# Optimization experiments

Measured on AMD Instinct MI355X. Metric: run time of the kernel, lower is better.

## Reference

```python
import math
import jax, jax.numpy as jnp
import numpy as np

PHI = (1.0 + math.sqrt(5.0)) / 2.0
B, S, E, H, L = 2, 2048, 1024, 16, 5
DH = E // H


def setup_inputs() -> dict:
    key = jax.random.key(0)
    ks = jax.random.split(key, 16)
    rn = lambda k, sh, sc=0.02: jax.random.normal(k, sh, jnp.float32) * sc
    return {
        'x': jax.random.normal(ks[0], (B, S, E), jnp.float32),
        'consciousness_levels': jax.random.uniform(ks[1], (B, H), jnp.float32),
        'Wc': rn(ks[2], (L, E, E)), 'bc': jnp.zeros((L, E), jnp.float32),
        'Wf': rn(ks[3], (L, E, H)), 'bf': jnp.zeros((L, H), jnp.float32),
        'Wq': rn(ks[4], (E, E)), 'bq': jnp.zeros((E,), jnp.float32),
        'Wk': rn(ks[5], (E, E)), 'bk': jnp.zeros((E,), jnp.float32),
        'Wv': rn(ks[6], (E, E)), 'bv': jnp.zeros((E,), jnp.float32),
        'Wo': rn(ks[7], (E, E)), 'bo': jnp.zeros((E,), jnp.float32),
        'Wc1': rn(ks[8], (2 * DH, E)), 'bc1': jnp.zeros((E,), jnp.float32),
        'Wc2': rn(ks[9], (E, 1)), 'bc2': jnp.zeros((1,), jnp.float32),
        'gate': jax.random.normal(ks[10], (L, H), jnp.float32) / math.sqrt(H),
        'phi_phase': PHI * jnp.arange(H, dtype=jnp.float32),
        'ln_g': jnp.ones((E,), jnp.float32), 'ln_b': jnp.zeros((E,), jnp.float32),
    }


def reference(x, consciousness_levels, Wc, bc, Wf, bf, Wq, bq, Wk, bk, Wv, bv,
              Wo, bo, Wc1, bc1, Wc2, bc2, gate, phi_phase, ln_g, ln_b):
    b, s, e = x.shape
    l, _, h = Wf.shape
    dh = e // h
    # per-level consciousness scalar: consciousness_levels[:, level % num_heads] -> [B, L]
    cl = consciousness_levels[:, jnp.arange(l) % h]
    # consciousness-enhanced features: mean over L of (x @ Wc_l + bc_l) * cl[:, l]
    feat = jnp.einsum('bse,leo->lbso', x, Wc) + bc[:, None, None, :]   # [L,B,S,E]
    ce = jnp.mean(feat * cl.T[:, :, None, None], axis=0)                # [B,S,E]
    # QKV projections (spectral_norm linears; normalized weights supplied directly)
    Q = (ce @ Wq + bq).reshape(b, s, h, dh).transpose(0, 2, 1, 3)       # [B,H,S,Dh]
    K = (ce @ Wk + bk).reshape(b, s, h, dh).transpose(0, 2, 1, 3)
    V = (ce @ Wv + bv).reshape(b, s, h, dh).transpose(0, 2, 1, 3)
    scores = jnp.einsum('bhsd,bhtd->bhst', Q, K) / math.sqrt(dh)        # [B,H,S,S]
    # phi-harmonic phase modulation (scalar per (B,H), averaged over levels)
    pooled = ce.mean(axis=1)                                            # [B,E]
    freq = jnp.einsum('be,leh->lbh', pooled, Wf) + bf[:, None, :]       # [L,B,H]
    phase = jnp.sin(phi_phase[None, None, :] * freq * cl.T[:, :, None]).mean(axis=0)  # [B,H]
    scores = scores + 0.1 * phase[:, :, None, None]
    # quantum coherence gate per (B,H): sigmoid MLP on pooled Q/K head features
    ci = jnp.concatenate([Q.mean(axis=2), K.mean(axis=2)], axis=-1)     # [B,H,2*Dh]
    cw = jax.nn.sigmoid(jax.nn.gelu(ci @ Wc1 + bc1, approximate=False) @ Wc2 + bc2)  # [B,H,1]
    scores = scores * (1.0 + cw[..., None])
    aw = jax.nn.softmax(scores, axis=-1)
    # consciousness gating on attention weights, then re-softmax
    gw = jax.nn.softmax(gate, axis=1)                                   # [L,H]
    factor = jnp.prod(1.0 + 0.1 * cl[:, :, None] * gw[None, :, :], axis=1)  # [B,H]
    aw = jax.nn.softmax(aw * factor[:, :, None, None], axis=-1)
    attended = jnp.einsum('bhst,bhtd->bhsd', aw, V)
    out = attended.transpose(0, 2, 1, 3).reshape(b, s, e) @ Wo + bo
    y = x + out  # dropout is identity in eval
    mu = y.mean(axis=-1, keepdims=True)
    var = ((y - mu) ** 2).mean(axis=-1, keepdims=True)
    return (y - mu) / jnp.sqrt(var + 1e-5) * ln_g + ln_b
```

## Files before the change

### kernel.cpp

```cpp
#include <hip/hip_runtime.h>
#include <math.h>

#define BB 2
#define SS 2048
#define EE 1024
#define HH 16
#define LL 5
#define DH 64
#define QS (3 * 1024)

typedef __attribute__((ext_vector_type(8))) short bf16x8;
typedef __attribute__((ext_vector_type(4))) float f32x4;

__device__ __forceinline__ unsigned short f2bf(float f) {
  unsigned u = __float_as_uint(f);
  u += 0x7fffu + ((u >> 16) & 1u);
  return (unsigned short)(u >> 16);
}
__device__ __forceinline__ float bf2f(unsigned short u) {
  return __uint_as_float((unsigned)u << 16);
}
__device__ __forceinline__ f32x4 mfma16(bf16x8 a, bf16x8 b, f32x4 c) {
  return __builtin_amdgcn_mfma_f32_16x16x32_bf16(a, b, c, 0, 0, 0);
}
__device__ __forceinline__ unsigned cvtpk(float a, float b) {
  unsigned r;
  asm("v_cvt_pk_bf16_f32 %0, %1, %2" : "=v"(r) : "v"(a), "v"(b));
  return r;
}
__device__ __forceinline__ void gload16(const unsigned short* g, unsigned short* l) {
  __builtin_amdgcn_global_load_lds(
      (const __attribute__((address_space(1))) void*)g,
      (__attribute__((address_space(3))) void*)l, 16, 0, 0);
}

__global__ void prep_pack(const float* __restrict__ cons, const float* __restrict__ gate,
                          const float* __restrict__ bc,
                          const float* __restrict__ bq, const float* __restrict__ bk,
                          const float* __restrict__ bv,
                          float* __restrict__ beff, float* __restrict__ bqkv,
                          float* __restrict__ factor) {
  int i = blockIdx.x * 256 + threadIdx.x;
  if (i == 0) {
    float gw[LL][HH];
    for (int l = 0; l < LL; ++l) {
      float mx = -1e30f;
      for (int h = 0; h < HH; ++h) mx = fmaxf(mx, gate[l * HH + h]);
      float s = 0.f;
      for (int h = 0; h < HH; ++h) { gw[l][h] = expf(gate[l * HH + h] - mx); s += gw[l][h]; }
      for (int h = 0; h < HH; ++h) gw[l][h] /= s;
    }
    for (int b = 0; b < BB; ++b)
      for (int h = 0; h < HH; ++h) {
        float f = 1.f;
        for (int l = 0; l < LL; ++l) f *= 1.f + 0.1f * cons[b * HH + l] * gw[l][h];
        factor[b * HH + h] = f;
      }
  }
  if (i < BB * EE) {
    int b = i >> 10, e = i & 1023;
    float a = 0.f;
    #pragma unroll
    for (int l = 0; l < LL; ++l) a += cons[b * HH + l] * bc[l * EE + e];
    beff[i] = a * (1.f / LL);
  } else {
    int j = i - BB * EE;
    float v = (j < EE) ? bq[j] : (j < 2 * EE) ? bk[j - EE] : bv[j - 2 * EE];
    bqkv[j] = v;
  }
}

__global__ __launch_bounds__(256) void wceffT_kernel(const float* __restrict__ Wc,
                                                     const float* __restrict__ cons,
                                                     unsigned short* __restrict__ Wt) {
  int o0 = blockIdx.x * 64, e0 = blockIdx.y * 64, b = blockIdx.z;
  __shared__ float t[64][69];
  int tid = threadIdx.x;
  float w[LL];
  #pragma unroll
  for (int l = 0; l < LL; ++l) w[l] = cons[b * HH + l] * (1.f / LL);
  #pragma unroll
  for (int i = 0; i < 4; ++i) {
    int idx = tid + i * 256;
    int r = idx >> 4, c4 = idx & 15;
    float4 acc = {0.f, 0.f, 0.f, 0.f};
    #pragma unroll
    for (int l = 0; l < LL; ++l) {
      float4 v = *(const float4*)&Wc[(long)l * EE * EE + (long)(e0 + r) * EE + o0 + c4 * 4];
      acc.x += w[l] * v.x; acc.y += w[l] * v.y; acc.z += w[l] * v.z; acc.w += w[l] * v.w;
    }
    t[r][c4 * 4 + 0] = acc.x; t[r][c4 * 4 + 1] = acc.y;
    t[r][c4 * 4 + 2] = acc.z; t[r][c4 * 4 + 3] = acc.w;
  }
  __syncthreads();
  #pragma unroll
  for (int i = 0; i < 2; ++i) {
    int idx = tid + i * 256;
    int o = idx >> 3, ech = idx & 7;
    unsigned short u[8];
    #pragma unroll
    for (int j = 0; j < 8; ++j) u[j] = f2bf(t[ech * 8 + j][o]);
    unsigned short* dst = Wt + (long)b * EE * EE + (long)(o0 + o) * EE + e0 + ech * 8;
    *(ushort4*)&dst[0] = *(ushort4*)&u[0];
    *(ushort4*)&dst[4] = *(ushort4*)&u[4];
  }
}

__global__ __launch_bounds__(256) void wT4_kernel(
    const float* __restrict__ W0, const float* __restrict__ W1,
    const float* __restrict__ W2, const float* __restrict__ W3,
    unsigned short* __restrict__ Wqkvt, unsigned short* __restrict__ Wot) {
  int z = blockIdx.z;
  const float* W = (z == 0) ? W0 : (z == 1) ? W1 : (z == 2) ? W2 : W3;
  unsigned short* Wt = (z < 3) ? (Wqkvt + (size_t)z * EE * EE) : Wot;
  int o0 = blockIdx.x * 64, e0 = blockIdx.y * 64;
  __shared__ float t[64][69];
  int tid = threadIdx.x;
  #pragma unroll
  for (int i = 0; i < 4; ++i) {
    int idx = tid + i * 256;
    int r = idx >> 4, c4 = idx & 15;
    float4 v = *(const float4*)&W[(long)(e0 + r) * EE + o0 + c4 * 4];
    t[r][c4 * 4 + 0] = v.x; t[r][c4 * 4 + 1] = v.y;
    t[r][c4 * 4 + 2] = v.z; t[r][c4 * 4 + 3] = v.w;
  }
  __syncthreads();
  #pragma unroll
  for (int i = 0; i < 2; ++i) {
    int idx = tid + i * 256;
    int o = idx >> 3, ech = idx & 7;
    unsigned short u[8];
    #pragma unroll
    for (int j = 0; j < 8; ++j) u[j] = f2bf(t[ech * 8 + j][o]);
    unsigned short* dst = Wt + (long)(o0 + o) * EE + e0 + ech * 8;
    *(ushort4*)&dst[0] = *(ushort4*)&u[0];
    *(ushort4*)&dst[4] = *(ushort4*)&u[4];
  }
}

__global__ void cvt_bf_kernel(const float* __restrict__ in, unsigned short* __restrict__ out) {
  long i = (long)blockIdx.x * 256 + threadIdx.x;
  float4 a = ((const float4*)in)[i * 2];
  float4 b = ((const float4*)in)[i * 2 + 1];
  ushort4 u0 = make_ushort4(f2bf(a.x), f2bf(a.y), f2bf(a.z), f2bf(a.w));
  ushort4 u1 = make_ushort4(f2bf(b.x), f2bf(b.y), f2bf(b.z), f2bf(b.w));
  ((ushort4*)out)[i * 2] = u0;
  ((ushort4*)out)[i * 2 + 1] = u1;
}

template <int OUTBF>
__global__ __launch_bounds__(256) void gemm128(
    const unsigned short* __restrict__ A, const unsigned short* __restrict__ Bt,
    const float* __restrict__ bias, void* __restrict__ C,
    int N, int K, long As_z, long Ws_z, long Bs_z, long Cs_z) {
  int flat = blockIdx.x + gridDim.x * (blockIdx.y + gridDim.y * blockIdx.z);
  int nwg = gridDim.x * gridDim.y * gridDim.z;
  flat = (flat & 7) * (nwg >> 3) + (flat >> 3);
  int nt_ = flat % gridDim.x;
  int rest = flat / gridDim.x;
  int mt_ = rest % gridDim.y;
  int z = rest / gridDim.y;

  const unsigned short* Ab = A + z * As_z + (long)mt_ * 128 * K;
  const unsigned short* Bb = Bt + z * Ws_z + (long)nt_ * 128 * K;
  const float* bb = bias + z * Bs_z + nt_ * 128;

  __shared__ __align__(16) unsigned short As[2][128 * 64];
  __shared__ __align__(16) unsigned short Bs[2][128 * 64];
  int tid = threadIdx.x;
  int w = tid >> 6, lane = tid & 63, c = lane & 15, g = lane >> 4;
  int wrow = (w >> 1) * 64, wcol = (w & 1) * 64;

  #define STG128(srcp, dstbuf, kt)                                             \
    {                                                                          \
      const unsigned short* s_ = (srcp) + (kt) * 64;                           \
      _Pragma("unroll") for (int j = 0; j < 4; ++j) {                          \
        int idx = tid + j * 256;                                               \
        int row = idx >> 3, ch = idx & 7;                                      \
        gload16(s_ + (long)row * K + ((ch ^ (row & 7)) << 3),                  \
                &dstbuf[(idx & ~63) * 8 + (lane)*8]);                          \
      }                                                                        \
    }

  f32x4 acc[4][4];
  #pragma unroll
  for (int mi = 0; mi < 4; ++mi)
    #pragma unroll
    for (int ni = 0; ni < 4; ++ni) acc[mi][ni] = {0.f, 0.f, 0.f, 0.f};

  int nk = K >> 6;
  STG128(Ab, As[0], 0) STG128(Bb, Bs[0], 0)
  __syncthreads();
  int buf = 0;
  for (int kt = 0; kt < nk; ++kt) {
    if (kt + 1 < nk) { STG128(Ab, As[buf ^ 1], kt + 1) STG128(Bb, Bs[buf ^ 1], kt + 1) }
    #pragma unroll
    for (int kk = 0; kk < 2; ++kk) {
      bf16x8 af[4], bfv[4];
      #pragma unroll
      for (int mi = 0; mi < 4; ++mi) {
        int row = wrow + mi * 16 + c;
        af[mi] = *(const bf16x8*)&As[buf][row * 64 + ((((kk << 2) + g) ^ (row & 7)) << 3)];
      }
      #pragma unroll
      for (int ni = 0; ni < 4; ++ni) {
        int row = wcol + ni * 16 + c;
        bfv[ni] = *(const bf16x8*)&Bs[buf][row * 64 + ((((kk << 2) + g) ^ (row & 7)) << 3)];
      }
      #pragma unroll
      for (int mi = 0; mi < 4; ++mi)
        #pragma unroll
        for (int ni = 0; ni < 4; ++ni)
          acc[mi][ni] = mfma16(af[mi], bfv[ni], acc[mi][ni]);
    }
    __syncthreads();
    buf ^= 1;
  }

  float bval[4];
  #pragma unroll
  for (int ni = 0; ni < 4; ++ni) bval[ni] = bb[wcol + ni * 16 + c];
  #pragma unroll
  for (int mi = 0; mi < 4; ++mi)
    #pragma unroll
    for (int ni = 0; ni < 4; ++ni) {
      long col = (long)nt_ * 128 + wcol + ni * 16 + c;
      #pragma unroll
      for (int r = 0; r < 4; ++r) {
        long row = (long)mt_ * 128 + wrow + mi * 16 + g * 4 + r;
        float v = acc[mi][ni][r] + bval[ni];
        if (OUTBF)
          ((unsigned short*)C)[z * Cs_z + row * N + col] = f2bf(v);
        else
          ((float*)C)[z * Cs_z + row * N + col] = v;
      }
    }
  #undef STG128
}

__global__ void mean2_kernel(const unsigned short* __restrict__ QKVb,
                             float* __restrict__ Qm, float* __restrict__ Km) {
  int z = blockIdx.z;
  const unsigned short* in = QKVb + z * EE;
  float* out = z ? Km : Qm;
  int e = blockIdx.x * 256 + threadIdx.x;
  int b = e >> 10, ee = e & 1023;
  int s0 = blockIdx.y * 128;
  const unsigned short* p = in + ((long)b * SS + s0) * QS + ee;
  float acc = 0.f;
  for (int i = 0; i < 128; ++i) acc += bf2f(p[(long)i * QS]);
  atomicAdd(&out[e], acc * (1.f / SS));
}

__global__ __launch_bounds__(256) void cw_kernel(
    const float* __restrict__ Qm, const float* __restrict__ Km,
    const float* __restrict__ Wc1, const float* __restrict__ bc1,
    const float* __restrict__ Wc2, const float* __restrict__ bc2,
    float* __restrict__ alpha) {
  int bh = blockIdx.x, b = bh / HH, h = bh % HH;
  __shared__ float ci[128];
  __shared__ float pr[4];
  int tid = threadIdx.x;
  if (tid < 64) ci[tid] = Qm[b * EE + h * DH + tid];
  else if (tid < 128) ci[tid] = Km[b * EE + h * DH + (tid - 64)];
  __syncthreads();
  float part = 0.f;
  for (int j = tid; j < EE; j += 256) {
    float acc = bc1[j];
    #pragma unroll 8
    for (int i = 0; i < 128; ++i) acc += ci[i] * Wc1[i * EE + j];
    float ge = 0.5f * acc * (1.f + erff(acc * 0.70710678118654752f));
    part += ge * Wc2[j];
  }
  #pragma unroll
  for (int off = 32; off; off >>= 1) part += __shfl_xor(part, off);
  if ((tid & 63) == 0) pr[tid >> 6] = part;
  __syncthreads();
  if (tid == 0) {
    float tot = pr[0] + pr[1] + pr[2] + pr[3] + bc2[0];
    float cw = 1.f / (1.f + expf(-tot));
    alpha[bh] = 1.f + cw;
  }
}

__global__ __launch_bounds__(256) void repack_vT(const unsigned short* __restrict__ Vh,
                                                 unsigned short* __restrict__ Vt) {
  int st = blockIdx.x, h = blockIdx.y, b = blockIdx.z;
  __shared__ unsigned short tile[64][66];
  int tid = threadIdx.x;
  const unsigned short* src = Vh + ((long)(b * SS) + st * 64) * QS + h * 64;
  #pragma unroll
  for (int i = 0; i < 2; ++i) {
    int idx = tid + i * 256;
    int s = idx >> 3, ch = idx & 7;
    #pragma unroll
    for (int j = 0; j < 8; ++j) tile[s][ch * 8 + j] = src[(long)s * QS + ch * 8 + j];
  }
  __syncthreads();
  unsigned short* dst = Vt + ((long)(b * HH + h) * 64) * SS + st * 64;
  #pragma unroll
  for (int i = 0; i < 2; ++i) {
    int idx = tid + i * 256;
    int d = idx >> 3, sch = idx & 7;
    unsigned short u[8];
    #pragma unroll
    for (int j = 0; j < 8; ++j) u[j] = tile[sch * 8 + j][d];
    *(ushort4*)&dst[(long)d * SS + sch * 8] = *(ushort4*)&u[0];
    *(ushort4*)&dst[(long)d * SS + sch * 8 + 4] = *(ushort4*)&u[4];
  }
}

__global__ __launch_bounds__(256) void vsum_kernel(const unsigned short* __restrict__ Vt,
                                                   float* __restrict__ Vsum) {
  int row = blockIdx.x * 4 + (threadIdx.x >> 6);
  int lane = threadIdx.x & 63;
  const unsigned short* p = Vt + (long)row * SS + lane * 32;
  float acc = 0.f;
  #pragma unroll
  for (int i = 0; i < 4; ++i) {
    uint4 v = *(const uint4*)(p + i * 8);
    unsigned arr[4] = {v.x, v.y, v.z, v.w};
    #pragma unroll
    for (int j = 0; j < 4; ++j) {
      acc += __uint_as_float(arr[j] << 16);
      acc += __uint_as_float(arr[j] & 0xffff0000u);
    }
  }
  #pragma unroll
  for (int off = 32; off; off >>= 1) acc += __shfl_xor(acc, off);
  if (lane == 0) Vsum[row] = acc;
}

__global__ __launch_bounds__(256, 4) void attn_lin(
    const unsigned short* __restrict__ QKV,
    const unsigned short* __restrict__ Vt,
    const float* __restrict__ alpha,
    float* __restrict__ Np0, float* __restrict__ Np1,
    float* __restrict__ m1p) {
  int flat = blockIdx.x;
  flat = (flat & 7) * 128 + (flat >> 3);
  int qt = flat & 15, h = (flat >> 4) & 15, b = (flat >> 8) & 1, part = flat >> 9;
  int bh = b * HH + h;
  int tid = threadIdx.x;
  int l = tid & 63, w = tid >> 6, c = l & 15, g = l >> 4;
  __shared__ __align__(16) unsigned short kbuf[4096];
  __shared__ __align__(16) unsigned short vbuf[4096];
  __shared__ __align__(16) unsigned short pws[4][1024];

  const unsigned short* Kb_ =
      QKV + (long)b * SS * QS + EE + h * 64 + (long)part * 1024 * QS;
  const unsigned short* Vb_ = Vt + (long)bh * 64 * SS + part * 1024;
  float* Np = part ? Np1 : Np0;
  const float scaleE = alpha[bh] * 0.125f;
  const f32x4 zero4 = {0.f, 0.f, 0.f, 0.f};

  bf16x8 qf[2][2];
  {
    const unsigned short* qp =
        QKV + ((long)b * SS + qt * 128 + w * 32 + c) * QS + h * 64;
    qf[0][0] = *(const bf16x8*)(qp + 8 * g);
    qf[0][1] = *(const bf16x8*)(qp + 32 + 8 * g);
    qf[1][0] = *(const bf16x8*)(qp + 16 * QS + 8 * g);
    qf[1][1] = *(const bf16x8*)(qp + 16 * QS + 32 + 8 * g);
  }

  int off1 = tid, off2 = tid + 256;
  int r1 = off1 >> 3, ch1 = ((off1 & 7) ^ (r1 & 7)) << 3;
  int r2 = off2 >> 3, ch2 = ((off2 & 7) ^ (r2 & 7)) << 3;
  const unsigned short* kg1 = Kb_ + (long)r1 * QS + ch1;
  const unsigned short* kg2 = Kb_ + (long)r2 * QS + ch2;
  const unsigned short* vg1 = Vb_ + (long)r1 * SS + ch1;
  const unsigned short* vg2 = Vb_ + (long)r2 * SS + ch2;

  uint4 ks1 = *(const uint4*)kg1, ks2 = *(const uint4*)kg2;
  uint4 vs1 = *(const uint4*)vg1, vs2 = *(const uint4*)vg2;
  kg1 += (long)64 * QS; kg2 += (long)64 * QS; vg1 += 64; vg2 += 64;
  *(uint4*)&kbuf[off1 * 8] = ks1; *(uint4*)&kbuf[off2 * 8] = ks2;
  *(uint4*)&vbuf[off1 * 8] = vs1; *(uint4*)&vbuf[off2 * 8] = vs2;
  __syncthreads();

  f32x4 N1[4][2];
  #pragma unroll
  for (int d = 0; d < 4; ++d) { N1[d][0] = zero4; N1[d][1] = zero4; }
  float m1l0 = 0.f, m1l1 = 0.f;
  unsigned short* pw = pws[w];

  const int NT2 = 16;
  for (int t = 0; t < NT2; ++t) {
    if (t + 1 < NT2) {
      ks1 = *(const uint4*)kg1; ks2 = *(const uint4*)kg2;
      vs1 = *(const uint4*)vg1; vs2 = *(const uint4*)vg2;
      kg1 += (long)64 * QS; kg2 += (long)64 * QS; vg1 += 64; vg2 += 64;
    }
    __builtin_amdgcn_s_setprio(1);
    #pragma unroll
    for (int half = 0; half < 2; ++half) {
      #pragma unroll
      for (int mth = 0; mth < 2; ++mth) {
        int mt = half * 2 + mth;
        int r = mt * 16 + c;
        bf16x8 a0 = *(const bf16x8*)&kbuf[r * 64 + ((g ^ (r & 7)) << 3)];
        bf16x8 a1 = *(const bf16x8*)&kbuf[r * 64 + (((4 + g) ^ (r & 7)) << 3)];
        int ch = 2 * mth + (g >> 1);
        #pragma unroll
        for (int qb = 0; qb < 2; ++qb) {
          f32x4 s = mfma16(a0, qf[qb][0], zero4);
          s = mfma16(a1, qf[qb][1], s);
          float u0 = __expf(s[0] * scaleE), u1 = __expf(s[1] * scaleE);
          float u2 = __expf(s[2] * scaleE), u3 = __expf(s[3] * scaleE);
          if (qb == 0) m1l0 += (u0 + u1) + (u2 + u3);
          else         m1l1 += (u0 + u1) + (u2 + u3);
          int row = qb * 16 + c;
          int swz = (ch ^ (row & 3) ^ ((row >> 2) & 3)) & 3;
          *(uint2*)&pw[row * 32 + (swz << 3) + ((g & 1) << 2)] =
              make_uint2(cvtpk(u0, u1), cvtpk(u2, u3));
        }
      }
      bf16x8 pf[2];
      #pragma unroll
      for (int qb = 0; qb < 2; ++qb) {
        int row = qb * 16 + c;
        int swz = (g ^ (row & 3) ^ ((row >> 2) & 3)) & 3;
        pf[qb] = *(const bf16x8*)&pw[row * 32 + (swz << 3)];
      }
      #pragma unroll
      for (int dblk = 0; dblk < 4; ++dblk) {
        int r = dblk * 16 + c;
        bf16x8 v = *(const bf16x8*)&vbuf[r * 64 + (((half * 4 + g) ^ (r & 7)) << 3)];
        N1[dblk][0] = mfma16(v, pf[0], N1[dblk][0]);
        N1[dblk][1] = mfma16(v, pf[1], N1[dblk][1]);
      }
    }
    __builtin_amdgcn_s_setprio(0);
    __syncthreads();
    if (t + 1 < NT2) {
      *(uint4*)&kbuf[off1 * 8] = ks1; *(uint4*)&kbuf[off2 * 8] = ks2;
      *(uint4*)&vbuf[off1 * 8] = vs1; *(uint4*)&vbuf[off2 * 8] = vs2;
    }
    __syncthreads();
  }

  m1l0 += __shfl_xor(m1l0, 16); m1l0 += __shfl_xor(m1l0, 32);
  m1l1 += __shfl_xor(m1l1, 16); m1l1 += __shfl_xor(m1l1, 32);
  if (l < 16) {
    long mb = ((long)(part * BB + b) * HH + h) * SS + qt * 128 + w * 32;
    m1p[mb + c] = m1l0;
    m1p[mb + 16 + c] = m1l1;
  }

  #pragma unroll
  for (int qb = 0; qb < 2; ++qb) {
    float* np = Np + ((long)b * SS + qt * 128 + w * 32 + qb * 16 + c) * EE + h * 64;
    #pragma unroll
    for (int dblk = 0; dblk < 4; ++dblk) {
      float4 o = {N1[dblk][qb][0], N1[dblk][qb][1], N1[dblk][qb][2], N1[dblk][qb][3]};
      *(float4*)&np[dblk * 16 + 4 * g] = o;
    }
  }
}

__global__ __launch_bounds__(256) void attn_combine(
    const float* __restrict__ Np0, const float* __restrict__ Np1,
    const float* __restrict__ m1p, const float* __restrict__ Vsum,
    const float* __restrict__ factor, unsigned short* __restrict__ att) {
  int row = blockIdx.x;
  int b = row >> 11, s = row & 2047;
  int e0 = threadIdx.x * 4;
  int h = e0 >> 6, d = e0 & 63;
  int bh = b * HH + h;
  float m1 = m1p[((long)b * HH + h) * SS + s] +
             m1p[((long)(BB + b) * HH + h) * SS + s];
  float fac = factor[bh];
  float c1 = fac / m1;
  float invden = 1.f / ((float)SS + fac);
  long base = (long)row * EE + e0;
  float4 n0 = *(const float4*)&Np0[base];
  float4 n1 = *(const float4*)&Np1[base];
  float4 vs = *(const float4*)&Vsum[bh * 64 + d];
  float o0 = (vs.x + c1 * (n0.x + n1.x)) * invden;
  float o1 = (vs.y + c1 * (n0.y + n1.y)) * invden;
  float o2 = (vs.z + c1 * (n0.z + n1.z)) * invden;
  float o3 = (vs.w + c1 * (n0.w + n1.w)) * invden;
  *(uint2*)&att[base] = make_uint2(cvtpk(o0, o1), cvtpk(o2, o3));
}

__global__ __launch_bounds__(256) void ln_kernel(
    const float* __restrict__ x, const float* __restrict__ proj,
    const float* __restrict__ g, const float* __restrict__ bb,
    float* __restrict__ out) {
  long row = blockIdx.x;
  const float* xp = x + row * EE;
  const float* pp = proj + row * EE;
  int tid = threadIdx.x;
  float v[4];
  float s = 0.f;
  __shared__ float r1[4], r2[4];
  #pragma unroll
  for (int i = 0; i < 4; ++i) {
    int e = tid + i * 256;
    v[i] = xp[e] + pp[e];
    s += v[i];
  }
  #pragma unroll
  for (int off = 32; off; off >>= 1) s += __shfl_xor(s, off);
  if ((tid & 63) == 0) r1[tid >> 6] = s;
  __syncthreads();
  float mean = (r1[0] + r1[1] + r1[2] + r1[3]) * (1.f / EE);
  float s2 = 0.f;
  #pragma unroll
  for (int i = 0; i < 4; ++i) { float d = v[i] - mean; s2 += d * d; }
  #pragma unroll
  for (int off = 32; off; off >>= 1) s2 += __shfl_xor(s2, off);
  if ((tid & 63) == 0) r2[tid >> 6] = s2;
  __syncthreads();
  float rstd = rsqrtf((r2[0] + r2[1] + r2[2] + r2[3]) * (1.f / EE) + 1e-5f);
  #pragma unroll
  for (int i = 0; i < 4; ++i) {
    int e = tid + i * 256;
    out[row * EE + e] = (v[i] - mean) * rstd * g[e] + bb[e];
  }
}

extern "C" void kernel_launch(void* const* d_in, const int* in_sizes, int n_in,
                              void* d_out, int out_size, void* d_ws, size_t ws_size,
                              hipStream_t stream) {
  (void)in_sizes; (void)n_in; (void)out_size; (void)ws_size;
  const float* x    = (const float*)d_in[0];
  const float* cons = (const float*)d_in[1];
  const float* Wc   = (const float*)d_in[2];
  const float* bc   = (const float*)d_in[3];
  const float* Wq   = (const float*)d_in[6];
  const float* bq   = (const float*)d_in[7];
  const float* Wk   = (const float*)d_in[8];
  const float* bk   = (const float*)d_in[9];
  const float* Wv   = (const float*)d_in[10];
  const float* bv   = (const float*)d_in[11];
  const float* Wo   = (const float*)d_in[12];
  const float* bo   = (const float*)d_in[13];
  const float* Wc1  = (const float*)d_in[14];
  const float* bc1  = (const float*)d_in[15];
  const float* Wc2  = (const float*)d_in[16];
  const float* bc2  = (const float*)d_in[17];
  const float* gate = (const float*)d_in[18];
  const float* ln_g = (const float*)d_in[20];
  const float* ln_b = (const float*)d_in[21];
  float* out = (float*)d_out;

  const size_t MSZ = (size_t)BB * SS * EE;
  float* p = (float*)d_ws;
  float* beff = p;  p += BB * EE;
  float* factor = p; p += 32;
  float* alpha  = p; p += 32;
  float* Qm   = p;  p += BB * EE;
  float* Km   = p;  p += BB * EE;
  float* bqkv = p;  p += QS;
  float* Vsum = p;  p += BB * EE;
  float* proj = p;  p += MSZ;
  unsigned short* q = (unsigned short*)p;
  unsigned short* xbf  = q;  q += MSZ;
  unsigned short* cebf = q;  q += MSZ;
  unsigned short* QKVb = q;  q += 3 * MSZ;
  unsigned short* Vt   = q;  q += MSZ;
  unsigned short* attb = q;  q += MSZ;
  unsigned short* Weft = q;  q += (size_t)BB * EE * EE;
  unsigned short* Wqkvt= q;  q += (size_t)3 * EE * EE;
  unsigned short* Wot  = q;  q += (size_t)EE * EE;
  float* m1p = (float*)q;    q += 2 * 2 * BB * HH * SS;
  float* Np0 = (float*)xbf;
  float* Np1 = proj;

  prep_pack<<<(BB * EE + QS) / 256, 256, 0, stream>>>(cons, gate, bc, bq, bk, bv,
                                                      beff, bqkv, factor);
  wceffT_kernel<<<dim3(16, 16, 2), 256, 0, stream>>>(Wc, cons, Weft);
  wT4_kernel<<<dim3(16, 16, 4), 256, 0, stream>>>(Wq, Wk, Wv, Wo, Wqkvt, Wot);
  cvt_bf_kernel<<<MSZ / 8 / 256, 256, 0, stream>>>(x, xbf);

  dim3 cgrid(EE / 128, SS / 128, BB);
  gemm128<1><<<cgrid, 256, 0, stream>>>(xbf, Weft, beff, cebf, EE, EE,
                                        (long)SS * EE, (long)EE * EE, EE, (long)SS * EE);
  dim3 qgrid(QS / 128, SS / 128, BB);
  gemm128<1><<<qgrid, 256, 0, stream>>>(cebf, Wqkvt, bqkv, QKVb, QS, EE,
                                        (long)SS * EE, 0, 0, (long)SS * QS);

  hipMemsetAsync(Qm, 0, (size_t)2 * BB * EE * sizeof(float), stream);
  mean2_kernel<<<dim3((BB * EE) / 256, SS / 128, 2), 256, 0, stream>>>(QKVb, Qm, Km);
  cw_kernel<<<BB * HH, 256, 0, stream>>>(Qm, Km, Wc1, bc1, Wc2, bc2, alpha);

  repack_vT<<<dim3(SS / 64, HH, BB), 256, 0, stream>>>(QKVb + 2 * EE, Vt);
  vsum_kernel<<<(BB * EE) / 4, 256, 0, stream>>>(Vt, Vsum);

  attn_lin<<<1024, 256, 0, stream>>>(QKVb, Vt, alpha, Np0, Np1, m1p);
  attn_combine<<<BB * SS, 256, 0, stream>>>(Np0, Np1, m1p, Vsum, factor, attb);

  gemm128<0><<<cgrid, 256, 0, stream>>>(attb, Wot, bo, proj, EE, EE,
                                        (long)SS * EE, 0, 0, (long)SS * EE);
  ln_kernel<<<BB * SS, 256, 0, stream>>>(x, proj, ln_g, ln_b, out);
}
```

Measured before the change: 216.8 us.

## Double-buffer attention K/V tiles with direct global-to-LDS loads; fuse V sum into repack

The attention kernel now keeps two LDS buffers for K and V and issues direct global-to-LDS loads (gload16) for the next tile while computing on the current one. This drops the register staging and one of the two barriers per iteration. Separately, the V column sum is folded into the transpose kernel using atomics, which removes a launch, and the memset is widened to zero the moved Vsum buffer. The trade-off is double the K/V LDS footprint, which may reduce occupancy, plus atomic contention on Vsum.

```diff
diff --git a/kernel.cpp b/kernel.cpp
--- a/kernel.cpp
+++ b/kernel.cpp
@@ -284,7 +284,8 @@
 }
 
 __global__ __launch_bounds__(256) void repack_vT(const unsigned short* __restrict__ Vh,
-                                                 unsigned short* __restrict__ Vt) {
+                                                 unsigned short* __restrict__ Vt,
+                                                 float* __restrict__ Vsum) {
   int st = blockIdx.x, h = blockIdx.y, b = blockIdx.z;
   __shared__ unsigned short tile[64][66];
   int tid = threadIdx.x;
@@ -308,27 +309,13 @@
     *(ushort4*)&dst[(long)d * SS + sch * 8] = *(ushort4*)&u[0];
     *(ushort4*)&dst[(long)d * SS + sch * 8 + 4] = *(ushort4*)&u[4];
   }
-}
-
-__global__ __launch_bounds__(256) void vsum_kernel(const unsigned short* __restrict__ Vt,
-                                                   float* __restrict__ Vsum) {
-  int row = blockIdx.x * 4 + (threadIdx.x >> 6);
-  int lane = threadIdx.x & 63;
-  const unsigned short* p = Vt + (long)row * SS + lane * 32;
-  float acc = 0.f;
-  #pragma unroll
-  for (int i = 0; i < 4; ++i) {
-    uint4 v = *(const uint4*)(p + i * 8);
-    unsigned arr[4] = {v.x, v.y, v.z, v.w};
-    #pragma unroll
-    for (int j = 0; j < 4; ++j) {
-      acc += __uint_as_float(arr[j] << 16);
-      acc += __uint_as_float(arr[j] & 0xffff0000u);
-    }
-  }
-  #pragma unroll
-  for (int off = 32; off; off >>= 1) acc += __shfl_xor(acc, off);
-  if (lane == 0) Vsum[row] = acc;
+  {
+    int d = tid & 63, quarter = tid >> 6;
+    float part = 0.f;
+    #pragma unroll
+    for (int j = 0; j < 16; ++j) part += bf2f(tile[quarter * 16 + j][d]);
+    atomicAdd(&Vsum[((long)(b * HH + h)) * 64 + d], part);
+  }
 }
 
 __global__ __launch_bounds__(256, 4) void attn_lin(
@@ -343,8 +330,8 @@
   int bh = b * HH + h;
   int tid = threadIdx.x;
   int l = tid & 63, w = tid >> 6, c = l & 15, g = l >> 4;
-  __shared__ __align__(16) unsigned short kbuf[4096];
-  __shared__ __align__(16) unsigned short vbuf[4096];
+  __shared__ __align__(16) unsigned short kbuf[2][4096];
+  __shared__ __align__(16) unsigned short vbuf[2][4096];
   __shared__ __align__(16) unsigned short pws[4][1024];
 
   const unsigned short* Kb_ =
@@ -372,11 +359,11 @@
   const unsigned short* vg1 = Vb_ + (long)r1 * SS + ch1;
   const unsigned short* vg2 = Vb_ + (long)r2 * SS + ch2;
 
-  uint4 ks1 = *(const uint4*)kg1, ks2 = *(const uint4*)kg2;
-  uint4 vs1 = *(const uint4*)vg1, vs2 = *(const uint4*)vg2;
+  gload16(kg1, &kbuf[0][off1 * 8]);
+  gload16(kg2, &kbuf[0][off2 * 8]);
+  gload16(vg1, &vbuf[0][off1 * 8]);
+  gload16(vg2, &vbuf[0][off2 * 8]);
   kg1 += (long)64 * QS; kg2 += (long)64 * QS; vg1 += 64; vg2 += 64;
-  *(uint4*)&kbuf[off1 * 8] = ks1; *(uint4*)&kbuf[off2 * 8] = ks2;
-  *(uint4*)&vbuf[off1 * 8] = vs1; *(uint4*)&vbuf[off2 * 8] = vs2;
   __syncthreads();
 
   f32x4 N1[4][2];
@@ -385,13 +372,18 @@
   float m1l0 = 0.f, m1l1 = 0.f;
   unsigned short* pw = pws[w];
 
+  int buf = 0;
   const int NT2 = 16;
   for (int t = 0; t < NT2; ++t) {
     if (t + 1 < NT2) {
-      ks1 = *(const uint4*)kg1; ks2 = *(const uint4*)kg2;
-      vs1 = *(const uint4*)vg1; vs2 = *(const uint4*)vg2;
+      gload16(kg1, &kbuf[buf ^ 1][off1 * 8]);
+      gload16(kg2, &kbuf[buf ^ 1][off2 * 8]);
+      gload16(vg1, &vbuf[buf ^ 1][off1 * 8]);
+      gload16(vg2, &vbuf[buf ^ 1][off2 * 8]);
       kg1 += (long)64 * QS; kg2 += (long)64 * QS; vg1 += 64; vg2 += 64;
     }
+    const unsigned short* kb = kbuf[buf];
+    const unsigned short* vb = vbuf[buf];
     __builtin_amdgcn_s_setprio(1);
     #pragma unroll
     for (int half = 0; half < 2; ++half) {
@@ -399,8 +391,8 @@
       for (int mth = 0; mth < 2; ++mth) {
         int mt = half * 2 + mth;
         int r = mt * 16 + c;
-        bf16x8 a0 = *(const bf16x8*)&kbuf[r * 64 + ((g ^ (r & 7)) << 3)];
-        bf16x8 a1 = *(const bf16x8*)&kbuf[r * 64 + (((4 + g) ^ (r & 7)) << 3)];
+        bf16x8 a0 = *(const bf16x8*)&kb[r * 64 + ((g ^ (r & 7)) << 3)];
+        bf16x8 a1 = *(const bf16x8*)&kb[r * 64 + (((4 + g) ^ (r & 7)) << 3)];
         int ch = 2 * mth + (g >> 1);
         #pragma unroll
         for (int qb = 0; qb < 2; ++qb) {
@@ -426,18 +418,14 @@
       #pragma unroll
       for (int dblk = 0; dblk < 4; ++dblk) {
         int r = dblk * 16 + c;
-        bf16x8 v = *(const bf16x8*)&vbuf[r * 64 + (((half * 4 + g) ^ (r & 7)) << 3)];
+        bf16x8 v = *(const bf16x8*)&vb[r * 64 + (((half * 4 + g) ^ (r & 7)) << 3)];
         N1[dblk][0] = mfma16(v, pf[0], N1[dblk][0]);
         N1[dblk][1] = mfma16(v, pf[1], N1[dblk][1]);
       }
     }
     __builtin_amdgcn_s_setprio(0);
     __syncthreads();
-    if (t + 1 < NT2) {
-      *(uint4*)&kbuf[off1 * 8] = ks1; *(uint4*)&kbuf[off2 * 8] = ks2;
-      *(uint4*)&vbuf[off1 * 8] = vs1; *(uint4*)&vbuf[off2 * 8] = vs2;
-    }
-    __syncthreads();
+    buf ^= 1;
   }
 
   m1l0 += __shfl_xor(m1l0, 16); m1l0 += __shfl_xor(m1l0, 32);
@@ -553,8 +541,8 @@
   float* alpha  = p; p += 32;
   float* Qm   = p;  p += BB * EE;
   float* Km   = p;  p += BB * EE;
+  float* Vsum = p;  p += BB * EE;
   float* bqkv = p;  p += QS;
-  float* Vsum = p;  p += BB * EE;
   float* proj = p;  p += MSZ;
   unsigned short* q = (unsigned short*)p;
   unsigned short* xbf  = q;  q += MSZ;
@@ -582,12 +570,11 @@
   gemm128<1><<<qgrid, 256, 0, stream>>>(cebf, Wqkvt, bqkv, QKVb, QS, EE,
                                         (long)SS * EE, 0, 0, (long)SS * QS);
 
-  hipMemsetAsync(Qm, 0, (size_t)2 * BB * EE * sizeof(float), stream);
+  hipMemsetAsync(Qm, 0, (size_t)3 * BB * EE * sizeof(float), stream);
   mean2_kernel<<<dim3((BB * EE) / 256, SS / 128, 2), 256, 0, stream>>>(QKVb, Qm, Km);
   cw_kernel<<<BB * HH, 256, 0, stream>>>(Qm, Km, Wc1, bc1, Wc2, bc2, alpha);
 
-  repack_vT<<<dim3(SS / 64, HH, BB), 256, 0, stream>>>(QKVb + 2 * EE, Vt);
-  vsum_kernel<<<(BB * EE) / 4, 256, 0, stream>>>(Vt, Vsum);
+  repack_vT<<<dim3(SS / 64, HH, BB), 256, 0, stream>>>(QKVb + 2 * EE, Vt, Vsum);
 
   attn_lin<<<1024, 256, 0, stream>>>(QKVb, Vt, alpha, Np0, Np1, m1p);
   attn_combine<<<BB * SS, 256, 0, stream>>>(Np0, Np1, m1p, Vsum, factor, attb);
```

Result: no change. 216.9 us (+0.1%).

## Fuse V transpose into QKV GEMM epilogue and derive Q/K means from ce mean

Applied to the files above, without the earlier changes.

The QKV GEMM now writes the V columns directly in transposed per-head layout, which removes the separate repack_vT kernel and its extra pass over V. The Q/K head means are no longer obtained by reducing the large QKV output. Instead the mean of ce is computed once, and the projection through the bf16 Wq/Wk rows happens inside cw_kernel, using linearity of the mean. The transposed epilogue stores are strided and may coalesce less well. The mean is now taken before bf16 rounding of Q/K, which slightly changes numerics.

```diff
diff --git a/kernel.cpp b/kernel.cpp
--- a/kernel.cpp
+++ b/kernel.cpp
@@ -148,10 +148,11 @@
   ((ushort4*)out)[i * 2 + 1] = u1;
 }
 
-template <int OUTBF>
+template <int OUTBF, int VSPLIT>
 __global__ __launch_bounds__(256) void gemm128(
     const unsigned short* __restrict__ A, const unsigned short* __restrict__ Bt,
     const float* __restrict__ bias, void* __restrict__ C,
+    unsigned short* __restrict__ VtOut,
     int N, int K, long As_z, long Ws_z, long Bs_z, long Cs_z) {
   int flat = blockIdx.x + gridDim.x * (blockIdx.y + gridDim.y * blockIdx.z);
   int nwg = gridDim.x * gridDim.y * gridDim.z;
@@ -220,40 +221,57 @@
   float bval[4];
   #pragma unroll
   for (int ni = 0; ni < 4; ++ni) bval[ni] = bb[wcol + ni * 16 + c];
-  #pragma unroll
-  for (int mi = 0; mi < 4; ++mi)
-    #pragma unroll
-    for (int ni = 0; ni < 4; ++ni) {
-      long col = (long)nt_ * 128 + wcol + ni * 16 + c;
-      #pragma unroll
-      for (int r = 0; r < 4; ++r) {
-        long row = (long)mt_ * 128 + wrow + mi * 16 + g * 4 + r;
-        float v = acc[mi][ni][r] + bval[ni];
-        if (OUTBF)
-          ((unsigned short*)C)[z * Cs_z + row * N + col] = f2bf(v);
-        else
-          ((float*)C)[z * Cs_z + row * N + col] = v;
-      }
-    }
+  if (VSPLIT && nt_ >= 16) {
+    #pragma unroll
+    for (int mi = 0; mi < 4; ++mi) {
+      long s0 = (long)mt_ * 128 + wrow + mi * 16 + g * 4;
+      #pragma unroll
+      for (int ni = 0; ni < 4; ++ni) {
+        int vc = (nt_ - 16) * 128 + wcol + ni * 16 + c;
+        int bh = z * HH + (vc >> 6);
+        int d = vc & 63;
+        float a0 = acc[mi][ni][0] + bval[ni];
+        float a1 = acc[mi][ni][1] + bval[ni];
+        float a2 = acc[mi][ni][2] + bval[ni];
+        float a3 = acc[mi][ni][3] + bval[ni];
+        *(uint2*)&VtOut[((long)bh * 64 + d) * SS + s0] =
+            make_uint2(cvtpk(a0, a1), cvtpk(a2, a3));
+      }
+    }
+  } else {
+    #pragma unroll
+    for (int mi = 0; mi < 4; ++mi)
+      #pragma unroll
+      for (int ni = 0; ni < 4; ++ni) {
+        long col = (long)nt_ * 128 + wcol + ni * 16 + c;
+        #pragma unroll
+        for (int r = 0; r < 4; ++r) {
+          long row = (long)mt_ * 128 + wrow + mi * 16 + g * 4 + r;
+          float v = acc[mi][ni][r] + bval[ni];
+          if (OUTBF)
+            ((unsigned short*)C)[z * Cs_z + row * N + col] = f2bf(v);
+          else
+            ((float*)C)[z * Cs_z + row * N + col] = v;
+        }
+      }
+  }
   #undef STG128
 }
 
-__global__ void mean2_kernel(const unsigned short* __restrict__ QKVb,
-                             float* __restrict__ Qm, float* __restrict__ Km) {
-  int z = blockIdx.z;
-  const unsigned short* in = QKVb + z * EE;
-  float* out = z ? Km : Qm;
+__global__ void mean_ce_kernel(const unsigned short* __restrict__ cebf,
+                               float* __restrict__ cemean) {
   int e = blockIdx.x * 256 + threadIdx.x;
   int b = e >> 10, ee = e & 1023;
   int s0 = blockIdx.y * 128;
-  const unsigned short* p = in + ((long)b * SS + s0) * QS + ee;
+  const unsigned short* p = cebf + ((long)b * SS + s0) * EE + ee;
   float acc = 0.f;
-  for (int i = 0; i < 128; ++i) acc += bf2f(p[(long)i * QS]);
-  atomicAdd(&out[e], acc * (1.f / SS));
+  for (int i = 0; i < 128; ++i) acc += bf2f(p[(long)i * EE]);
+  atomicAdd(&cemean[e], acc * (1.f / SS));
 }
 
 __global__ __launch_bounds__(256) void cw_kernel(
-    const float* __restrict__ Qm, const float* __restrict__ Km,
+    const float* __restrict__ cemean, const unsigned short* __restrict__ Wqkvt,
+    const float* __restrict__ bqkv,
     const float* __restrict__ Wc1, const float* __restrict__ bc1,
     const float* __restrict__ Wc2, const float* __restrict__ bc2,
     float* __restrict__ alpha) {
@@ -261,8 +279,25 @@
   __shared__ float ci[128];
   __shared__ float pr[4];
   int tid = threadIdx.x;
-  if (tid < 64) ci[tid] = Qm[b * EE + h * DH + tid];
-  else if (tid < 128) ci[tid] = Km[b * EE + h * DH + (tid - 64)];
+  if (tid < 128) {
+    int j = tid;
+    int col = h * 64 + (j & 63);
+    const unsigned short* wrow =
+        Wqkvt + ((j < 64) ? 0 : (size_t)EE * EE) + (long)col * EE;
+    float bias = bqkv[((j < 64) ? 0 : EE) + col];
+    const float* cm = cemean + b * EE;
+    float acc = 0.f;
+    for (int k = 0; k < EE; k += 8) {
+      uint4 v = *(const uint4*)&wrow[k];
+      unsigned arr[4] = {v.x, v.y, v.z, v.w};
+      #pragma unroll
+      for (int jj = 0; jj < 4; ++jj) {
+        acc += cm[k + 2 * jj] * bf2f((unsigned short)(arr[jj] & 0xffffu));
+        acc += cm[k + 2 * jj + 1] * bf2f((unsigned short)(arr[jj] >> 16));
+      }
+    }
+    ci[j] = acc + bias;
+  }
   __syncthreads();
   float part = 0.f;
   for (int j = tid; j < EE; j += 256) {
@@ -280,33 +315,6 @@
     float tot = pr[0] + pr[1] + pr[2] + pr[3] + bc2[0];
     float cw = 1.f / (1.f + expf(-tot));
     alpha[bh] = 1.f + cw;
-  }
-}
-
-__global__ __launch_bounds__(256) void repack_vT(const unsigned short* __restrict__ Vh,
-                                                 unsigned short* __restrict__ Vt) {
-  int st = blockIdx.x, h = blockIdx.y, b = blockIdx.z;
-  __shared__ unsigned short tile[64][66];
-  int tid = threadIdx.x;
-  const unsigned short* src = Vh + ((long)(b * SS) + st * 64) * QS + h * 64;
-  #pragma unroll
-  for (int i = 0; i < 2; ++i) {
-    int idx = tid + i * 256;
-    int s = idx >> 3, ch = idx & 7;
-    #pragma unroll
-    for (int j = 0; j < 8; ++j) tile[s][ch * 8 + j] = src[(long)s * QS + ch * 8 + j];
-  }
-  __syncthreads();
-  unsigned short* dst = Vt + ((long)(b * HH + h) * 64) * SS + st * 64;
-  #pragma unroll
-  for (int i = 0; i < 2; ++i) {
-    int idx = tid + i * 256;
-    int d = idx >> 3, sch = idx & 7;
-    unsigned short u[8];
-    #pragma unroll
-    for (int j = 0; j < 8; ++j) u[j] = tile[sch * 8 + j][d];
-    *(ushort4*)&dst[(long)d * SS + sch * 8] = *(ushort4*)&u[0];
-    *(ushort4*)&dst[(long)d * SS + sch * 8 + 4] = *(ushort4*)&u[4];
   }
 }
 
@@ -551,10 +559,9 @@
   float* beff = p;  p += BB * EE;
   float* factor = p; p += 32;
   float* alpha  = p; p += 32;
-  float* Qm   = p;  p += BB * EE;
-  float* Km   = p;  p += BB * EE;
+  float* cemean = p; p += BB * EE;
+  float* Vsum = p;  p += BB * EE;
   float* bqkv = p;  p += QS;
-  float* Vsum = p;  p += BB * EE;
   float* proj = p;  p += MSZ;
   unsigned short* q = (unsigned short*)p;
   unsigned short* xbf  = q;  q += MSZ;
@@ -576,23 +583,25 @@
   cvt_bf_kernel<<<MSZ / 8 / 256, 256, 0, stream>>>(x, xbf);
 
   dim3 cgrid(EE / 128, SS / 128, BB);
-  gemm128<1><<<cgrid, 256, 0, stream>>>(xbf, Weft, beff, cebf, EE, EE,
-                                        (long)SS * EE, (long)EE * EE, EE, (long)SS * EE);
+  gemm128<1, 0><<<cgrid, 256, 0, stream>>>(xbf, Weft, beff, cebf, nullptr, EE, EE,
+                                           (long)SS * EE, (long)EE * EE, EE,
+                                           (long)SS * EE);
+
+  hipMemsetAsync(cemean, 0, (size_t)BB * EE * sizeof(float), stream);
+  mean_ce_kernel<<<dim3((BB * EE) / 256, SS / 128), 256, 0, stream>>>(cebf, cemean);
+
   dim3 qgrid(QS / 128, SS / 128, BB);
-  gemm128<1><<<qgrid, 256, 0, stream>>>(cebf, Wqkvt, bqkv, QKVb, QS, EE,
-                                        (long)SS * EE, 0, 0, (long)SS * QS);
-
-  hipMemsetAsync(Qm, 0, (size_t)2 * BB * EE * sizeof(float), stream);
-  mean2_kernel<<<dim3((BB * EE) / 256, SS / 128, 2), 256, 0, stream>>>(QKVb, Qm, Km);
-  cw_kernel<<<BB * HH, 256, 0, stream>>>(Qm, Km, Wc1, bc1, Wc2, bc2, alpha);
-
-  repack_vT<<<dim3(SS / 64, HH, BB), 256, 0, stream>>>(QKVb + 2 * EE, Vt);
+  gemm128<1, 1><<<qgrid, 256, 0, stream>>>(cebf, Wqkvt, bqkv, QKVb, Vt, QS, EE,
+                                           (long)SS * EE, 0, 0, (long)SS * QS);
+
+  cw_kernel<<<BB * HH, 256, 0, stream>>>(cemean, Wqkvt, bqkv, Wc1, bc1, Wc2, bc2,
+                                         alpha);
   vsum_kernel<<<(BB * EE) / 4, 256, 0, stream>>>(Vt, Vsum);
 
   attn_lin<<<1024, 256, 0, stream>>>(QKVb, Vt, alpha, Np0, Np1, m1p);
   attn_combine<<<BB * SS, 256, 0, stream>>>(Np0, Np1, m1p, Vsum, factor, attb);
 
-  gemm128<0><<<cgrid, 256, 0, stream>>>(attb, Wot, bo, proj, EE, EE,
-                                        (long)SS * EE, 0, 0, (long)SS * EE);
+  gemm128<0, 0><<<cgrid, 256, 0, stream>>>(attb, Wot, bo, proj, nullptr, EE, EE,
+                                           (long)SS * EE, 0, 0, (long)SS * EE);
   ln_kernel<<<BB * SS, 256, 0, stream>>>(x, proj, ln_g, ln_b, out);
 }
```

New measurement: 235.7 us. +8.7%, slower.
